# Performance work log

Measured on AMD Instinct MI355X. Metric: run time of the kernel, lower is better.

## Reference

```python
import jax, jax.numpy as jnp
import numpy as np

DECAY = 0.99
EPSILON = 1e-05
BETA = 0.25  # vq_commitment_beta


def setup_inputs() -> dict:
    key = jax.random.key(0)
    k1, k2, k3, k4 = jax.random.split(key, 4)
    N, dim, K = 32768, 512, 8192
    init_range = 1.0 / np.sqrt(dim)
    emb_w = jax.random.uniform(k3, (K, 2 * dim), dtype=jnp.float32,
                               minval=-init_range, maxval=init_range)
    return {
        "z_real": jax.random.normal(k1, (N, dim), dtype=jnp.float32),
        "z_imag": jax.random.normal(k2, (N, dim), dtype=jnp.float32),
        "emb_w": emb_w,
        "ema_cluster_size": jnp.zeros((K,), dtype=jnp.float32),
        "ema_w": emb_w.copy(),
    }


def reference(z_real, z_imag, emb_w, ema_cluster_size, ema_w):
    N, dim = z_real.shape
    K = emb_w.shape[0]
    z_flat = jnp.concatenate([z_real, z_imag], axis=-1)  # [N, 2*dim]

    # squared euclidean distances [N, K]
    x_sq = jnp.sum(z_flat * z_flat, axis=1, keepdims=True)
    y_sq = jnp.sum(emb_w * emb_w, axis=1)
    d = jnp.maximum(x_sq + y_sq - 2.0 * (z_flat @ emb_w.T), 0.0)
    indices = jnp.argmin(d, axis=-1)  # [N]
    z_q = emb_w[indices]              # [N, 2*dim]

    # EMA codebook update (training-mode buffer math, no grads)
    n_total = jnp.zeros((K,), z_flat.dtype).at[indices].add(1.0)
    new_cluster_size = ema_cluster_size * DECAY + (1.0 - DECAY) * n_total
    cs = new_cluster_size + EPSILON
    cs = cs + (cs < 1.0).astype(cs.dtype)
    dw = jnp.zeros((K, 2 * dim), z_flat.dtype).at[indices].add(z_flat)  # encodings.T @ z_flat
    new_ema_w = ema_w * DECAY + (1.0 - DECAY) * dw
    new_w = jnp.clip(new_ema_w / cs[:, None], -5.0, 5.0)

    loss_sample = BETA * jnp.mean((z_q - z_flat) ** 2, axis=-1)  # [N]

    # straight-through (forward value == z_q)
    z_q_st = z_flat + jax.lax.stop_gradient(z_q - z_flat)

    probs = n_total / N
    norm_entropy = -jnp.sum(probs * jnp.log(probs + 1e-10)) / np.log(float(K))

    z_q_r = z_q_st[..., :dim]
    z_q_i = z_q_st[..., dim:]
    return (z_q_r, z_q_i, loss_sample, indices, norm_entropy,
            new_w, new_cluster_size, new_ema_w)
```

## Files before the change

kernel.cpp:

```cpp
#include <hip/hip_runtime.h>
#include <hip/hip_bf16.h>

#define NROWS 32768
#define DIM   512
#define D2    1024
#define KCODE 8192
#define DECAYF 0.99f
#define OMD    0.01f
#define MARGIN 0.30f
#define CANDCAP 16
#define ZMAX 6.0f
#define IRANGE 0.04419417382415922f

typedef __attribute__((ext_vector_type(4))) float f32x4;
typedef __attribute__((ext_vector_type(4))) int   v4i;
typedef __attribute__((ext_vector_type(16))) int  i32x16;

#define WS_EMB8T   0u
#define WS_YSQ     8388608u
#define WS_NINT    8421376u
#define WS_ENT     8454144u
#define WS_CCOUNT  8454160u
#define WS_CAND    8585232u
#define WS_FIDX    10682384u
#define WS_OFF     10813456u
#define WS_CUR     10846224u
#define WS_ROWLIST 10878992u

#define OUT_ZQR  0
#define OUT_ZQI  16777216
#define OUT_LOSS 33554432
#define OUT_IDX  33587200
#define OUT_ENT  33619968
#define OUT_NEWW 33619969
#define OUT_NCS  42008577
#define OUT_NEMA 42016769

__device__ __forceinline__ float wredf(float v) {
    #pragma unroll
    for (int o = 32; o > 0; o >>= 1) v += __shfl_down(v, o, 64);
    return v;
}

__device__ __forceinline__ double wredd(double v) {
    #pragma unroll
    for (int o = 32; o > 0; o >>= 1) v += __shfl_down(v, o, 64);
    return __shfl(v, 0, 64);
}

__device__ __forceinline__ double ulp32_of(double v) {
    return scalbn(1.0, ilogb(v) - 23);
}

__device__ __forceinline__ void gload_lds16(const void* g, void* l) {
    __builtin_amdgcn_global_load_lds(
        (const __attribute__((address_space(1))) unsigned int*)(g),
        (__attribute__((address_space(3))) unsigned int*)(l), 16, 0, 0);
}

__device__ __forceinline__ int q4(float4 v, float s) {
    int a = (int)rintf(fminf(fmaxf(v.x * s, -127.f), 127.f));
    int b = (int)rintf(fminf(fmaxf(v.y * s, -127.f), 127.f));
    int c = (int)rintf(fminf(fmaxf(v.z * s, -127.f), 127.f));
    int d = (int)rintf(fminf(fmaxf(v.w * s, -127.f), 127.f));
    return (a & 255) | ((b & 255) << 8) | ((c & 255) << 16) | ((d & 255) << 24);
}

__global__ __launch_bounds__(256) void prep_emb(const float* __restrict__ emb,
                                                char* __restrict__ emb8t,
                                                float* __restrict__ ysq) {
    int wave = threadIdx.x >> 6, lane = threadIdx.x & 63;
    int k = blockIdx.x * 4 + wave;
    const float4* src = (const float4*)(emb + (size_t)k * D2);
    const float es = 127.0f / IRANGE;
    float s = 0.f;
    float4 v0 = src[lane * 4 + 0];
    float4 v1 = src[lane * 4 + 1];
    float4 v2 = src[lane * 4 + 2];
    float4 v3 = src[lane * 4 + 3];
    s += v0.x*v0.x + v0.y*v0.y + v0.z*v0.z + v0.w*v0.w;
    s += v1.x*v1.x + v1.y*v1.y + v1.z*v1.z + v1.w*v1.w;
    s += v2.x*v2.x + v2.y*v2.y + v2.z*v2.z + v2.w*v2.w;
    s += v3.x*v3.x + v3.y*v3.y + v3.z*v3.z + v3.w*v3.w;
    v4i pk; pk[0] = q4(v0, es); pk[1] = q4(v1, es); pk[2] = q4(v2, es); pk[3] = q4(v3, es);
    v4i* dst = (v4i*)(emb8t + (size_t)(k >> 5) * 32768 + (size_t)lane * 512 + (k & 31) * 16);
    *dst = pk;
    s = wredf(s);
    if (lane == 0) ysq[k] = s;
}

__global__ __launch_bounds__(256, 2) void argmin_gemm(
    const float* __restrict__ zr, const float* __restrict__ zi,
    const char* __restrict__ emb8t, const float* __restrict__ ysq,
    long long* __restrict__ pairs)
{
    __shared__ char bufs[2][32768];
    const int tid  = threadIdx.x;
    const int wave = tid >> 6, lane = tid & 63;
    const int colc = lane & 31;
    const int hh   = lane >> 5;
    const int rowblk = blockIdx.x >> 1;
    const int slice  = blockIdx.x & 1;

    const int arow = rowblk * 128 + wave * 32 + colc;
    const float zs = 127.0f / ZMAX;
    const float* zrp = zr + (size_t)arow * 512 + hh * 16;
    const float* zip = zi + (size_t)arow * 512 + hh * 16;
    v4i afrag[32];
    #pragma unroll
    for (int ft = 0; ft < 16; ++ft) {
        const float4* p = (const float4*)(zrp + ft * 32);
        v4i a; a[0] = q4(p[0], zs); a[1] = q4(p[1], zs); a[2] = q4(p[2], zs); a[3] = q4(p[3], zs);
        afrag[ft] = a;
    }
    #pragma unroll
    for (int ft = 0; ft < 16; ++ft) {
        const float4* p = (const float4*)(zip + ft * 32);
        v4i a; a[0] = q4(p[0], zs); a[1] = q4(p[1], zs); a[2] = q4(p[2], zs); a[3] = q4(p[3], zs);
        afrag[16 + ft] = a;
    }

    float tv0[16], tv1[16];
    int cpk[16];
    #pragma unroll
    for (int g = 0; g < 16; ++g) { tv0[g] = 3.4e38f; tv1[g] = 3.4e38f; cpk[g] = 0; }

    const char* gslice = emb8t + (size_t)slice * 128 * 32768;
    const float* yslice = ysq + slice * 4096;

#define STAGE(dstbuf, chunk_) do {                                               \
        const char* gb = gslice + (size_t)(chunk_) * 32768 + wave * 8192         \
                       + (size_t)lane * 16;                                      \
        char* lb = (dstbuf) + wave * 8192;                                       \
        _Pragma("unroll")                                                        \
        for (int q = 0; q < 8; ++q)                                              \
            gload_lds16(gb + q * 1024, lb + q * 1024);                           \
    } while (0)

    const float sfac = 2.0f * (ZMAX / 127.0f) * (IRANGE / 127.0f);
    const int boff = colc * 16 + hh * 512;

    STAGE(bufs[0], 0);
    __syncthreads();

    for (int c = 0; c < 128; ++c) {
        const int cur = c & 1;
        if (c + 1 < 128) STAGE(bufs[cur ^ 1], c + 1);

        const char* bb = &bufs[cur][0] + boff;
        i32x16 acc0, acc1;
        #pragma unroll
        for (int g = 0; g < 16; ++g) { acc0[g] = 0; acc1[g] = 0; }
        #pragma unroll
        for (int m = 0; m < 32; m += 2) {
            v4i b0 = *(const v4i*)(bb + (m    ) * 1024);
            v4i b1 = *(const v4i*)(bb + (m + 1) * 1024);
            acc0 = __builtin_amdgcn_mfma_i32_32x32x32_i8(afrag[m],     b0, acc0, 0, 0, 0);
            acc1 = __builtin_amdgcn_mfma_i32_32x32x32_i8(afrag[m + 1], b1, acc1, 0, 0, 0);
        }

        float ysv = yslice[c * 32 + colc];
        #pragma unroll
        for (int g = 0; g < 16; ++g) {
            float fdot = (float)(acc0[g] + acc1[g]);
            float sc = fmaf(-sfac, fdot, ysv);
            if (sc < tv1[g]) {
                bool b0 = sc < tv0[g];
                int cp = cpk[g];
                cpk[g] = b0 ? (((cp & 0xFF) << 8) | c) : ((cp & 0xFF) | (c << 8));
                float ov0 = tv0[g];
                tv1[g] = b0 ? ov0 : sc;
                tv0[g] = b0 ? sc : ov0;
            }
        }
        __syncthreads();
    }
#undef STAGE

    #pragma unroll
    for (int g = 0; g < 16; ++g) {
        int rloc = (g & 3) + 8 * (g >> 2) + 4 * hh;
        int rowg = rowblk * 128 + wave * 32 + rloc;
        size_t base = (size_t)rowg * 128 + slice * 64 + colc * 2;
        int cp = cpk[g];
        int code0 = slice * 4096 + (cp & 0xFF) * 32 + colc;
        int code1 = slice * 4096 + ((cp >> 8) & 0xFF) * 32 + colc;
        pairs[base + 0] = ((long long)(unsigned)code0 << 32) | (unsigned)__float_as_uint(tv0[g]);
        pairs[base + 1] = ((long long)(unsigned)code1 << 32) | (unsigned)__float_as_uint(tv1[g]);
    }
}

__global__ __launch_bounds__(256) void merge_rows(const long long* __restrict__ pairs,
                                                  int* __restrict__ cand,
                                                  int* __restrict__ ccount)
{
    int wave = threadIdx.x >> 6, lane = threadIdx.x & 63;
    int row = blockIdx.x * 4 + wave;
    const long long* pr = pairs + (size_t)row * 128;
    long long p0 = pr[lane];
    long long p1 = pr[64 + lane];
    float v0v = __uint_as_float((unsigned)p0);
    int   i0  = (int)(p0 >> 32);
    float v1v = __uint_as_float((unsigned)p1);
    int   i1  = (int)(p1 >> 32);
    float m = fminf(v0v, v1v);
    #pragma unroll
    for (int o = 32; o > 0; o >>= 1) m = fminf(m, __shfl_xor(m, o, 64));
    float lim = m + MARGIN;
    unsigned long long m0 = __ballot(v0v < lim);
    unsigned long long m1 = __ballot(v1v < lim);
    int t0 = __popcll(m0);
    int cnt = t0 + __popcll(m1);
    if (cnt > CANDCAP) cnt = CANDCAP;
    unsigned long long below = (lane == 63) ? 0xFFFFFFFFFFFFFFFFull >> 1
                                            : ((1ull << lane) - 1);
    if (v0v < lim) {
        int pos = __popcll(m0 & below);
        if (pos < CANDCAP) cand[(size_t)row * CANDCAP + pos] = i0;
    }
    if (v1v < lim) {
        int pos = t0 + __popcll(m1 & below);
        if (pos < CANDCAP) cand[(size_t)row * CANDCAP + pos] = i1;
    }
    if (lane == 0) ccount[row] = cnt;
}

__global__ __launch_bounds__(256) void cleanup(
    const float* __restrict__ zr, const float* __restrict__ zi,
    const float* __restrict__ emb, const int* __restrict__ cand,
    const int* __restrict__ ccount, int* __restrict__ fidx,
    int* __restrict__ nint, float* __restrict__ out)
{
    int wave = threadIdx.x >> 6, lane = threadIdx.x & 63;
    int r = blockIdx.x * 4 + wave;
    int cnt = ccount[r];
    int best = cand[r * CANDCAP];
    if (cnt > 1) {
        float zreg[16];
        double xs = 0.0;
        #pragma unroll
        for (int p = 0; p < 4; ++p) {
            int d4 = p * 64 + lane;
            const float4* zp = (d4 < 128) ? (const float4*)(zr + (size_t)r * 512)
                                          : ((const float4*)(zi + (size_t)r * 512) - 128);
            float4 zv = zp[d4];
            zreg[p * 4 + 0] = zv.x; zreg[p * 4 + 1] = zv.y;
            zreg[p * 4 + 2] = zv.z; zreg[p * 4 + 3] = zv.w;
            xs += (double)zv.x * zv.x + (double)zv.y * zv.y
                + (double)zv.z * zv.z + (double)zv.w * zv.w;
        }
        xs = wredd(xs);
        double uS = ulp32_of(xs);

        double bD = 1e300; int bi = 1 << 30;
        for (int i = 0; i < cnt; ++i) {
            int cdx = cand[r * CANDCAP + i];
            const float4* ep = (const float4*)(emb + (size_t)cdx * 1024);
            double ys = 0.0, tt = 0.0;
            #pragma unroll
            for (int p = 0; p < 4; ++p) {
                float4 ev = ep[p * 64 + lane];
                float p0 = ev.x * ev.x, p1 = ev.y * ev.y, p2 = ev.z * ev.z, p3 = ev.w * ev.w;
                ys += (double)p0 + (double)p1 + (double)p2 + (double)p3;
                tt += (double)zreg[p * 4 + 0] * (double)ev.x
                    + (double)zreg[p * 4 + 1] * (double)ev.y
                    + (double)zreg[p * 4 + 2] * (double)ev.z
                    + (double)zreg[p * 4 + 3] * (double)ev.w;
            }
            ys = wredd(ys);
            tt = wredd(tt);
            float y32 = (float)ys;
            float t32 = (float)tt;
            double dex = xs + ys - 2.0 * tt;
            double ud = ulp32_of(dex);
            double D = rint((double)y32 / uS) * uS - rint(2.0 * (double)t32 / ud) * ud;
            if (D < bD || (D == bD && cdx < bi)) { bD = D; bi = cdx; }
        }
        best = bi;
    }
    if (lane == 0) {
        fidx[r] = best;
        out[OUT_IDX + r] = (float)best;
        atomicAdd(nint + best, 1);
    }
}

__global__ __launch_bounds__(256) void scan_codes(const int* __restrict__ nint,
                                                  int* __restrict__ off,
                                                  int* __restrict__ cur) {
    __shared__ int part[256];
    int tid = threadIdx.x;
    int base = tid * 32;
    int loc[32];
    int s = 0;
    #pragma unroll
    for (int j = 0; j < 32; ++j) { loc[j] = s; s += nint[base + j]; }
    part[tid] = s;
    __syncthreads();
    for (int o = 1; o < 256; o <<= 1) {
        int t = (tid >= o) ? part[tid - o] : 0;
        __syncthreads();
        part[tid] += t;
        __syncthreads();
    }
    int excl = part[tid] - s;
    #pragma unroll
    for (int j = 0; j < 32; ++j) {
        off[base + j] = excl + loc[j];
        cur[base + j] = 0;
    }
}

__global__ __launch_bounds__(256) void fill_rows(const int* __restrict__ fidx,
                                                 const int* __restrict__ off,
                                                 int* __restrict__ cur,
                                                 int* __restrict__ rowlist) {
    int r = blockIdx.x * 256 + threadIdx.x;
    int idx = fidx[r];
    int pos = atomicAdd(cur + idx, 1);
    rowlist[off[idx] + pos] = r;
}

__global__ __launch_bounds__(256) void ema_update(
    const float* __restrict__ zr, const float* __restrict__ zi,
    const float* __restrict__ emaw, const float* __restrict__ emacs,
    const int* __restrict__ nint, const int* __restrict__ off,
    const int* __restrict__ rowlist, float* __restrict__ out,
    float* __restrict__ entacc)
{
    int k = blockIdx.x;
    int tid = threadIdx.x;
    int cnt = nint[k];
    int o0 = off[k];
    float ax = 0.f, ay = 0.f, az = 0.f, aw = 0.f;
    for (int i = 0; i < cnt; ++i) {
        int r = rowlist[o0 + i];
        float4 zv = (tid < 128) ? ((const float4*)(zr + (size_t)r * 512))[tid]
                                : ((const float4*)(zi + (size_t)r * 512))[tid - 128];
        ax += zv.x; ay += zv.y; az += zv.z; aw += zv.w;
    }
    float4 ew = ((const float4*)(emaw + (size_t)k * 1024))[tid];
    float4 nem;
    nem.x = DECAYF * ew.x + OMD * ax;
    nem.y = DECAYF * ew.y + OMD * ay;
    nem.z = DECAYF * ew.z + OMD * az;
    nem.w = DECAYF * ew.w + OMD * aw;
    ((float4*)(out + OUT_NEMA + (size_t)k * 1024))[tid] = nem;
    float ncs = DECAYF * emacs[k] + OMD * (float)cnt;
    float cs = ncs + 1e-5f;
    if (cs < 1.f) cs += 1.f;
    float inv = 1.f / cs;
    float4 w;
    w.x = fminf(fmaxf(nem.x * inv, -5.f), 5.f);
    w.y = fminf(fmaxf(nem.y * inv, -5.f), 5.f);
    w.z = fminf(fmaxf(nem.z * inv, -5.f), 5.f);
    w.w = fminf(fmaxf(nem.w * inv, -5.f), 5.f);
    ((float4*)(out + OUT_NEWW + (size_t)k * 1024))[tid] = w;
    if (tid == 0) {
        out[OUT_NCS + k] = ncs;
        float p = (float)cnt / 32768.f;
        atomicAdd(entacc, -p * logf(p + 1e-10f));
    }
}

__global__ void ent_fin(const float* __restrict__ entacc, float* __restrict__ out) {
    if (threadIdx.x == 0) out[OUT_ENT] = entacc[0] / logf(8192.f);
}

__global__ __launch_bounds__(256) void zq_loss(
    const float* __restrict__ zr, const float* __restrict__ zi,
    const float* __restrict__ emb, const int* __restrict__ fidx, float* __restrict__ out)
{
    int wave = threadIdx.x >> 6, lane = threadIdx.x & 63;
    int r = blockIdx.x * 4 + wave;
    int idx = fidx[r];
    const float4* ep = (const float4*)(emb + (size_t)idx * 1024);
    float acc = 0.f;
    #pragma unroll
    for (int p = 0; p < 4; ++p) {
        int d4 = p * 64 + lane;
        const float4* zp = (d4 < 128) ? (const float4*)(zr + (size_t)r * 512)
                                      : ((const float4*)(zi + (size_t)r * 512) - 128);
        float4 zv = zp[d4];
        float4 ev = ep[d4];
        float dx = ev.x - zv.x; acc += dx * dx;
        float dy = ev.y - zv.y; acc += dy * dy;
        float dz = ev.z - zv.z; acc += dz * dz;
        float dw = ev.w - zv.w; acc += dw * dw;
        float4* op = (d4 < 128) ? (float4*)(out + OUT_ZQR + (size_t)r * 512)
                                : ((float4*)(out + OUT_ZQI + (size_t)r * 512) - 128);
        op[d4] = ev;
    }
    acc = wredf(acc);
    if (lane == 0) out[OUT_LOSS + r] = 0.25f * acc * (1.f / 1024.f);
}

extern "C" void kernel_launch(void* const* d_in, const int* in_sizes, int n_in,
                              void* d_out, int out_size, void* d_ws, size_t ws_size,
                              hipStream_t stream)
{
    const float* zr    = (const float*)d_in[0];
    const float* zi    = (const float*)d_in[1];
    const float* emb   = (const float*)d_in[2];
    const float* emacs = (const float*)d_in[3];
    const float* emaw  = (const float*)d_in[4];
    float* out = (float*)d_out;
    char* ws = (char*)d_ws;

    char*  emb8t   = (char*)(ws + WS_EMB8T);
    float* ysq     = (float*)(ws + WS_YSQ);
    int*   nint    = (int*)(ws + WS_NINT);
    float* entacc  = (float*)(ws + WS_ENT);
    int*   ccount  = (int*)(ws + WS_CCOUNT);
    int*   cand    = (int*)(ws + WS_CAND);
    int*   fidx    = (int*)(ws + WS_FIDX);
    int*   off     = (int*)(ws + WS_OFF);
    int*   cur     = (int*)(ws + WS_CUR);
    int*   rowlist = (int*)(ws + WS_ROWLIST);
    long long* pairs = (long long*)out;

    hipMemsetAsync(ws + WS_NINT, 0, 32768 + 16, stream);

    prep_emb   <<<2048, 256, 0, stream>>>(emb, emb8t, ysq);
    argmin_gemm<<<512,  256, 0, stream>>>(zr, zi, emb8t, ysq, pairs);
    merge_rows <<<8192, 256, 0, stream>>>(pairs, cand, ccount);
    cleanup    <<<8192, 256, 0, stream>>>(zr, zi, emb, cand, ccount, fidx, nint, out);
    scan_codes <<<1,    256, 0, stream>>>(nint, off, cur);
    fill_rows  <<<128,  256, 0, stream>>>(fidx, off, cur, rowlist);
    ema_update <<<8192, 256, 0, stream>>>(zr, zi, emaw, emacs, nint, off, rowlist, out, entacc);
    ent_fin    <<<1,    64,  0, stream>>>(entacc, out);
    zq_loss    <<<8192, 256, 0, stream>>>(zr, zi, emb, fidx, out);
}
```

Baseline: 587.9 us.

## Widen argmin GEMM tiles, score in integer domain, fuse zq/loss into cleanup

The argmin GEMM now runs 512-thread blocks covering 256 rows, staging 64 codes per chunk. Each A fragment feeds two MFMAs, which halves the loop trips and barriers. Candidate scores are kept as integers: the codebook squared norms are pre-scaled and rounded, so the per-element float conversion and FMA go away, and the merge margin becomes an integer constant. The separate zq_loss kernel is folded into cleanup, which already loads z, so z is not read a second time and one launch is removed. The trade-offs are 128KB of LDS per block, which likely allows only one block per CU, and integer rounding of the norm term, which relies on the candidate margin still covering quantization error.

```diff
diff --git a/kernel.cpp b/kernel.cpp
--- a/kernel.cpp
+++ b/kernel.cpp
@@ -7,10 +7,10 @@
 #define KCODE 8192
 #define DECAYF 0.99f
 #define OMD    0.01f
-#define MARGIN 0.30f
 #define CANDCAP 16
 #define ZMAX 6.0f
 #define IRANGE 0.04419417382415922f
+#define MARGIN_I 9200
 
 typedef __attribute__((ext_vector_type(4))) float f32x4;
 typedef __attribute__((ext_vector_type(4))) int   v4i;
@@ -68,11 +68,12 @@
 
 __global__ __launch_bounds__(256) void prep_emb(const float* __restrict__ emb,
                                                 char* __restrict__ emb8t,
-                                                float* __restrict__ ysq) {
+                                                int* __restrict__ ysq) {
     int wave = threadIdx.x >> 6, lane = threadIdx.x & 63;
     int k = blockIdx.x * 4 + wave;
     const float4* src = (const float4*)(emb + (size_t)k * D2);
     const float es = 127.0f / IRANGE;
+    const float sfac_inv = 1.0f / (2.0f * (ZMAX / 127.0f) * (IRANGE / 127.0f));
     float s = 0.f;
     float4 v0 = src[lane * 4 + 0];
     float4 v1 = src[lane * 4 + 1];
@@ -86,15 +87,15 @@
     v4i* dst = (v4i*)(emb8t + (size_t)(k >> 5) * 32768 + (size_t)lane * 512 + (k & 31) * 16);
     *dst = pk;
     s = wredf(s);
-    if (lane == 0) ysq[k] = s;
-}
-
-__global__ __launch_bounds__(256, 2) void argmin_gemm(
+    if (lane == 0) ysq[k] = (int)rintf(s * sfac_inv);
+}
+
+__global__ __launch_bounds__(512, 2) void argmin_gemm(
     const float* __restrict__ zr, const float* __restrict__ zi,
-    const char* __restrict__ emb8t, const float* __restrict__ ysq,
+    const char* __restrict__ emb8t, const int* __restrict__ ysq,
     long long* __restrict__ pairs)
 {
-    __shared__ char bufs[2][32768];
+    __shared__ char bufs[2][65536];
     const int tid  = threadIdx.x;
     const int wave = tid >> 6, lane = tid & 63;
     const int colc = lane & 31;
@@ -102,7 +103,7 @@
     const int rowblk = blockIdx.x >> 1;
     const int slice  = blockIdx.x & 1;
 
-    const int arow = rowblk * 128 + wave * 32 + colc;
+    const int arow = rowblk * 256 + wave * 32 + colc;
     const float zs = 127.0f / ZMAX;
     const float* zrp = zr + (size_t)arow * 512 + hh * 16;
     const float* zip = zi + (size_t)arow * 512 + hh * 16;
@@ -120,16 +121,15 @@
         afrag[16 + ft] = a;
     }
 
-    float tv0[16], tv1[16];
-    int cpk[16];
-    #pragma unroll
-    for (int g = 0; g < 16; ++g) { tv0[g] = 3.4e38f; tv1[g] = 3.4e38f; cpk[g] = 0; }
+    int tv0[16], tv1[16], cpk[16];
+    #pragma unroll
+    for (int g = 0; g < 16; ++g) { tv0[g] = 0x7FFFFFFF; tv1[g] = 0x7FFFFFFF; cpk[g] = 0; }
 
     const char* gslice = emb8t + (size_t)slice * 128 * 32768;
-    const float* yslice = ysq + slice * 4096;
-
-#define STAGE(dstbuf, chunk_) do {                                               \
-        const char* gb = gslice + (size_t)(chunk_) * 32768 + wave * 8192         \
+    const int* yslice = ysq + slice * 4096;
+
+#define STAGE(dstbuf, c_) do {                                                   \
+        const char* gb = gslice + (size_t)(c_) * 65536 + wave * 8192             \
                        + (size_t)lane * 16;                                      \
         char* lb = (dstbuf) + wave * 8192;                                       \
         _Pragma("unroll")                                                        \
@@ -137,38 +137,47 @@
             gload_lds16(gb + q * 1024, lb + q * 1024);                           \
     } while (0)
 
-    const float sfac = 2.0f * (ZMAX / 127.0f) * (IRANGE / 127.0f);
     const int boff = colc * 16 + hh * 512;
 
     STAGE(bufs[0], 0);
     __syncthreads();
 
-    for (int c = 0; c < 128; ++c) {
+    for (int c = 0; c < 64; ++c) {
         const int cur = c & 1;
-        if (c + 1 < 128) STAGE(bufs[cur ^ 1], c + 1);
+        if (c + 1 < 64) STAGE(bufs[cur ^ 1], c + 1);
 
         const char* bb = &bufs[cur][0] + boff;
-        i32x16 acc0, acc1;
+        i32x16 accA, accB;
         #pragma unroll
-        for (int g = 0; g < 16; ++g) { acc0[g] = 0; acc1[g] = 0; }
+        for (int g = 0; g < 16; ++g) { accA[g] = 0; accB[g] = 0; }
         #pragma unroll
-        for (int m = 0; m < 32; m += 2) {
-            v4i b0 = *(const v4i*)(bb + (m    ) * 1024);
-            v4i b1 = *(const v4i*)(bb + (m + 1) * 1024);
-            acc0 = __builtin_amdgcn_mfma_i32_32x32x32_i8(afrag[m],     b0, acc0, 0, 0, 0);
-            acc1 = __builtin_amdgcn_mfma_i32_32x32x32_i8(afrag[m + 1], b1, acc1, 0, 0, 0);
+        for (int m = 0; m < 32; ++m) {
+            v4i bA = *(const v4i*)(bb + m * 1024);
+            v4i bB = *(const v4i*)(bb + m * 1024 + 32768);
+            accA = __builtin_amdgcn_mfma_i32_32x32x32_i8(afrag[m], bA, accA, 0, 0, 0);
+            accB = __builtin_amdgcn_mfma_i32_32x32x32_i8(afrag[m], bB, accB, 0, 0, 0);
         }
 
-        float ysv = yslice[c * 32 + colc];
+        int ysA = yslice[c * 64 + colc];
+        int ysB = yslice[c * 64 + 32 + colc];
+        const int idA = c * 2, idB = c * 2 + 1;
         #pragma unroll
         for (int g = 0; g < 16; ++g) {
-            float fdot = (float)(acc0[g] + acc1[g]);
-            float sc = fmaf(-sfac, fdot, ysv);
+            int sc = ysA - accA[g];
             if (sc < tv1[g]) {
                 bool b0 = sc < tv0[g];
                 int cp = cpk[g];
-                cpk[g] = b0 ? (((cp & 0xFF) << 8) | c) : ((cp & 0xFF) | (c << 8));
-                float ov0 = tv0[g];
+                cpk[g] = b0 ? (((cp & 0xFF) << 8) | idA) : ((cp & 0xFF) | (idA << 8));
+                int ov0 = tv0[g];
+                tv1[g] = b0 ? ov0 : sc;
+                tv0[g] = b0 ? sc : ov0;
+            }
+            sc = ysB - accB[g];
+            if (sc < tv1[g]) {
+                bool b0 = sc < tv0[g];
+                int cp = cpk[g];
+                cpk[g] = b0 ? (((cp & 0xFF) << 8) | idB) : ((cp & 0xFF) | (idB << 8));
+                int ov0 = tv0[g];
                 tv1[g] = b0 ? ov0 : sc;
                 tv0[g] = b0 ? sc : ov0;
             }
@@ -180,13 +189,13 @@
     #pragma unroll
     for (int g = 0; g < 16; ++g) {
         int rloc = (g & 3) + 8 * (g >> 2) + 4 * hh;
-        int rowg = rowblk * 128 + wave * 32 + rloc;
+        int rowg = rowblk * 256 + wave * 32 + rloc;
         size_t base = (size_t)rowg * 128 + slice * 64 + colc * 2;
         int cp = cpk[g];
         int code0 = slice * 4096 + (cp & 0xFF) * 32 + colc;
         int code1 = slice * 4096 + ((cp >> 8) & 0xFF) * 32 + colc;
-        pairs[base + 0] = ((long long)(unsigned)code0 << 32) | (unsigned)__float_as_uint(tv0[g]);
-        pairs[base + 1] = ((long long)(unsigned)code1 << 32) | (unsigned)__float_as_uint(tv1[g]);
+        pairs[base + 0] = ((long long)(unsigned)code0 << 32) | (unsigned)tv0[g];
+        pairs[base + 1] = ((long long)(unsigned)code1 << 32) | (unsigned)tv1[g];
     }
 }
 
@@ -199,14 +208,14 @@
     const long long* pr = pairs + (size_t)row * 128;
     long long p0 = pr[lane];
     long long p1 = pr[64 + lane];
-    float v0v = __uint_as_float((unsigned)p0);
-    int   i0  = (int)(p0 >> 32);
-    float v1v = __uint_as_float((unsigned)p1);
-    int   i1  = (int)(p1 >> 32);
-    float m = fminf(v0v, v1v);
-    #pragma unroll
-    for (int o = 32; o > 0; o >>= 1) m = fminf(m, __shfl_xor(m, o, 64));
-    float lim = m + MARGIN;
+    int v0v = (int)(unsigned)p0;
+    int i0  = (int)(p0 >> 32);
+    int v1v = (int)(unsigned)p1;
+    int i1  = (int)(p1 >> 32);
+    int m = min(v0v, v1v);
+    #pragma unroll
+    for (int o = 32; o > 0; o >>= 1) m = min(m, __shfl_xor(m, o, 64));
+    int lim = m + MARGIN_I;
     unsigned long long m0 = __ballot(v0v < lim);
     unsigned long long m1 = __ballot(v1v < lim);
     int t0 = __popcll(m0);
@@ -235,20 +244,22 @@
     int r = blockIdx.x * 4 + wave;
     int cnt = ccount[r];
     int best = cand[r * CANDCAP];
+
+    float zreg[16];
+    #pragma unroll
+    for (int p = 0; p < 4; ++p) {
+        int d4 = p * 64 + lane;
+        const float4* zp = (d4 < 128) ? (const float4*)(zr + (size_t)r * 512)
+                                      : ((const float4*)(zi + (size_t)r * 512) - 128);
+        float4 zv = zp[d4];
+        zreg[p * 4 + 0] = zv.x; zreg[p * 4 + 1] = zv.y;
+        zreg[p * 4 + 2] = zv.z; zreg[p * 4 + 3] = zv.w;
+    }
+
     if (cnt > 1) {
-        float zreg[16];
         double xs = 0.0;
         #pragma unroll
-        for (int p = 0; p < 4; ++p) {
-            int d4 = p * 64 + lane;
-            const float4* zp = (d4 < 128) ? (const float4*)(zr + (size_t)r * 512)
-                                          : ((const float4*)(zi + (size_t)r * 512) - 128);
-            float4 zv = zp[d4];
-            zreg[p * 4 + 0] = zv.x; zreg[p * 4 + 1] = zv.y;
-            zreg[p * 4 + 2] = zv.z; zreg[p * 4 + 3] = zv.w;
-            xs += (double)zv.x * zv.x + (double)zv.y * zv.y
-                + (double)zv.z * zv.z + (double)zv.w * zv.w;
-        }
+        for (int j = 0; j < 16; ++j) xs += (double)zreg[j] * (double)zreg[j];
         xs = wredd(xs);
         double uS = ulp32_of(xs);
 
@@ -278,9 +289,26 @@
         }
         best = bi;
     }
+
+    const float4* ep = (const float4*)(emb + (size_t)best * 1024);
+    float acc = 0.f;
+    #pragma unroll
+    for (int p = 0; p < 4; ++p) {
+        int d4 = p * 64 + lane;
+        float4 ev = ep[d4];
+        float dx = ev.x - zreg[p * 4 + 0]; acc += dx * dx;
+        float dy = ev.y - zreg[p * 4 + 1]; acc += dy * dy;
+        float dz = ev.z - zreg[p * 4 + 2]; acc += dz * dz;
+        float dw = ev.w - zreg[p * 4 + 3]; acc += dw * dw;
+        float4* op = (d4 < 128) ? (float4*)(out + OUT_ZQR + (size_t)r * 512)
+                                : ((float4*)(out + OUT_ZQI + (size_t)r * 512) - 128);
+        op[d4] = ev;
+    }
+    acc = wredf(acc);
     if (lane == 0) {
         fidx[r] = best;
         out[OUT_IDX + r] = (float)best;
+        out[OUT_LOSS + r] = 0.25f * acc * (1.f / 1024.f);
         atomicAdd(nint + best, 1);
     }
 }
@@ -367,34 +395,6 @@
     if (threadIdx.x == 0) out[OUT_ENT] = entacc[0] / logf(8192.f);
 }
 
-__global__ __launch_bounds__(256) void zq_loss(
-    const float* __restrict__ zr, const float* __restrict__ zi,
-    const float* __restrict__ emb, const int* __restrict__ fidx, float* __restrict__ out)
-{
-    int wave = threadIdx.x >> 6, lane = threadIdx.x & 63;
-    int r = blockIdx.x * 4 + wave;
-    int idx = fidx[r];
-    const float4* ep = (const float4*)(emb + (size_t)idx * 1024);
-    float acc = 0.f;
-    #pragma unroll
-    for (int p = 0; p < 4; ++p) {
-        int d4 = p * 64 + lane;
-        const float4* zp = (d4 < 128) ? (const float4*)(zr + (size_t)r * 512)
-                                      : ((const float4*)(zi + (size_t)r * 512) - 128);
-        float4 zv = zp[d4];
-        float4 ev = ep[d4];
-        float dx = ev.x - zv.x; acc += dx * dx;
-        float dy = ev.y - zv.y; acc += dy * dy;
-        float dz = ev.z - zv.z; acc += dz * dz;
-        float dw = ev.w - zv.w; acc += dw * dw;
-        float4* op = (d4 < 128) ? (float4*)(out + OUT_ZQR + (size_t)r * 512)
-                                : ((float4*)(out + OUT_ZQI + (size_t)r * 512) - 128);
-        op[d4] = ev;
-    }
-    acc = wredf(acc);
-    if (lane == 0) out[OUT_LOSS + r] = 0.25f * acc * (1.f / 1024.f);
-}
-
 extern "C" void kernel_launch(void* const* d_in, const int* in_sizes, int n_in,
                               void* d_out, int out_size, void* d_ws, size_t ws_size,
                               hipStream_t stream)
@@ -408,7 +408,7 @@
     char* ws = (char*)d_ws;
 
     char*  emb8t   = (char*)(ws + WS_EMB8T);
-    float* ysq     = (float*)(ws + WS_YSQ);
+    int*   ysq     = (int*)(ws + WS_YSQ);
     int*   nint    = (int*)(ws + WS_NINT);
     float* entacc  = (float*)(ws + WS_ENT);
     int*   ccount  = (int*)(ws + WS_CCOUNT);
@@ -422,12 +422,11 @@
     hipMemsetAsync(ws + WS_NINT, 0, 32768 + 16, stream);
 
     prep_emb   <<<2048, 256, 0, stream>>>(emb, emb8t, ysq);
-    argmin_gemm<<<512,  256, 0, stream>>>(zr, zi, emb8t, ysq, pairs);
+    argmin_gemm<<<256,  512, 0, stream>>>(zr, zi, emb8t, ysq, pairs);
     merge_rows <<<8192, 256, 0, stream>>>(pairs, cand, ccount);
     cleanup    <<<8192, 256, 0, stream>>>(zr, zi, emb, cand, ccount, fidx, nint, out);
     scan_codes <<<1,    256, 0, stream>>>(nint, off, cur);
     fill_rows  <<<128,  256, 0, stream>>>(fidx, off, cur, rowlist);
     ema_update <<<8192, 256, 0, stream>>>(zr, zi, emaw, emacs, nint, off, rowlist, out, entacc);
     ent_fin    <<<1,    64,  0, stream>>>(entacc, out);
-    zq_loss    <<<8192, 256, 0, stream>>>(zr, zi, emb, fidx, out);
-}
+}
```

Result: faster. 550.9 us (-6.3%).
